# Kernel tuning notes

Measured on AMD Instinct MI355X. Metric: run time of the kernel, lower is better.

## Reference

```python
import jax, jax.numpy as jnp
import numpy as np

D = 64
N = 262144


def _stack_four(A, B, C, Dm):
    return jnp.block([[A, B], [C, Dm]])


def setup_inputs() -> dict:
    key = jax.random.key(0)
    # Z: (2d+1, n+1) in-context prompt matrix
    Z = jax.random.normal(key, (2 * D + 1, N + 1), dtype=jnp.float32)
    # P: zeros with P[-1,-1] = 1 (selects last row)
    P = jnp.zeros((2 * D + 1, 2 * D + 1), dtype=jnp.float32).at[-1, -1].set(1.0)
    # Q: block matrix built from M1, M2, B as in TFLayer.__init__
    I = jnp.eye(D, dtype=jnp.float32)
    O = jnp.zeros((D, D), dtype=jnp.float32)
    M1 = _stack_four(-I, I, O, O)
    M2 = -M1
    Bm = _stack_four(I, O, O, O)  # C = eye(d), so C.T = I
    A = M2.T @ Bm @ M1            # (2d, 2d)
    Q = jnp.zeros((2 * D + 1, 2 * D + 1), dtype=jnp.float32).at[: 2 * D, : 2 * D].set(A)
    return {"Z": Z, "P": P, "Q": Q}


def reference(Z, P, Q):
    # next_Z = Z + (1/n) * P @ Z @ M @ Z.T @ Q @ Z
    # M = eye(n+1) with M[-1,-1] = 0, i.e. right-mult by M zeroes the last
    # column. We never materialize the (n+1, n+1) identity.
    n = Z.shape[1] - 1
    PZ = P @ Z                         # (2d+1, n+1)
    PZM = PZ.at[:, -1].set(0.0)        # apply M: zero last column
    S = PZM @ Z.T                      # (2d+1, 2d+1) -- the only big contraction
    upd = (S @ Q) @ Z                  # (2d+1, n+1)
    return Z + upd / n
```

## Files before the change

### kernel.cpp

```cpp
#include <hip/hip_runtime.h>

#define DD      64
#define ROWS    129
#define NCOLS   262145
#define NDOT    262144
#define DOTROWS 128
#define CHUNK   2048
#define NCHUNK  128

__global__ void k_dot(const float* __restrict__ Z, float* __restrict__ partials) {
    const int row   = blockIdx.x & (DOTROWS - 1);
    const int chunk = blockIdx.x >> 7;
    const long base = (long)chunk * CHUNK;
    const float* zr = Z + (long)row * NCOLS + base;
    const float* zl = Z + (long)128 * NCOLS + base;
    const int tid = threadIdx.x;

    float acc = 0.f;
#pragma unroll
    for (int k = 0; k < CHUNK / 256; ++k) {
        const int c = tid + k * 256;
        acc = fmaf(zr[c], zl[c], acc);
    }
#pragma unroll
    for (int off = 32; off; off >>= 1) acc += __shfl_down(acc, off, 64);
    __shared__ float s[4];
    if ((tid & 63) == 0) s[tid >> 6] = acc;
    __syncthreads();
    if (tid == 0) {
        partials[(long)row * NCHUNK + chunk] = s[0] + s[1] + s[2] + s[3];
    }
}

__global__ void k_matvec(const float* __restrict__ partials,
                         const float* __restrict__ Q,
                         float* __restrict__ t) {
    __shared__ float v[DOTROWS];
    const int tid = threadIdx.x;
    float s = 0.f;
    for (int c = 0; c < NCHUNK; ++c) s += partials[(long)tid * NCHUNK + c];
    v[tid] = s;
    __syncthreads();
    float acc = 0.f;
#pragma unroll 8
    for (int m = 0; m < DOTROWS; ++m) acc = fmaf(v[m], Q[m * ROWS + tid], acc);
    t[tid] = acc * (1.0f / (float)NDOT);
}

__global__ void k_update(const float* __restrict__ Z,
                         const float* __restrict__ t,
                         float* __restrict__ out) {
    __shared__ float ts[DOTROWS];
    const int tid = threadIdx.x;
    if (tid < DOTROWS) ts[tid] = t[tid];
    __syncthreads();

    const long c = (long)blockIdx.x * blockDim.x + tid;
    if (c >= NCOLS) return;

    float acc = 0.f;
#pragma unroll 8
    for (int j = 0; j < DOTROWS; ++j) {
        const float val = Z[(long)j * NCOLS + c];
        out[(long)j * NCOLS + c] = val;
        acc = fmaf(ts[j], val, acc);
    }
    const float zl = Z[(long)128 * NCOLS + c];
    out[(long)128 * NCOLS + c] = zl + acc;
}

extern "C" void kernel_launch(void* const* d_in, const int* in_sizes, int n_in,
                              void* d_out, int out_size, void* d_ws, size_t ws_size,
                              hipStream_t stream) {
    const float* Z = (const float*)d_in[0];
    const float* Q = (const float*)d_in[2];
    float* out = (float*)d_out;

    float* partials = (float*)d_ws;
    float* t        = partials + DOTROWS * NCHUNK;

    k_dot<<<DOTROWS * NCHUNK, 256, 0, stream>>>(Z, partials);
    k_matvec<<<1, DOTROWS, 0, stream>>>(partials, Q, t);
    k_update<<<(NCOLS + 255) / 256, 256, 0, stream>>>(Z, t, out);
}
```

Measured before the change: 280.2 us.

## Fuse identity-row copy into dot pass and parallelize matvec across blocks

```diff
diff --git a/kernel.cpp b/kernel.cpp
--- a/kernel.cpp
+++ b/kernel.cpp
@@ -8,20 +8,38 @@
 #define CHUNK   2048
 #define NCHUNK  128
 
-__global__ void k_dot(const float* __restrict__ Z, float* __restrict__ partials) {
+__global__ __launch_bounds__(256) void k_dot_copy(const float* __restrict__ Z,
+                                                  float* __restrict__ out,
+                                                  float* __restrict__ partials) {
     const int row   = blockIdx.x & (DOTROWS - 1);
     const int chunk = blockIdx.x >> 7;
     const long base = (long)chunk * CHUNK;
     const float* zr = Z + (long)row * NCOLS + base;
-    const float* zl = Z + (long)128 * NCOLS + base;
+    const float* zl = Z + (long)DOTROWS * NCOLS + base;
+    float* orow     = out + (long)row * NCOLS + base;
     const int tid = threadIdx.x;
+
+    __shared__ float szl[CHUNK];
+    const float4* zl4 = (const float4*)zl;
+#pragma unroll
+    for (int k = 0; k < CHUNK / 4 / 256; ++k) {
+        ((float4*)szl)[tid + k * 256] = zl4[tid + k * 256];
+    }
+    __syncthreads();
 
     float acc = 0.f;
 #pragma unroll
     for (int k = 0; k < CHUNK / 256; ++k) {
         const int c = tid + k * 256;
-        acc = fmaf(zr[c], zl[c], acc);
+        const float v = zr[c];
+        __builtin_nontemporal_store(v, &orow[c]);
+        acc = fmaf(v, szl[c], acc);
     }
+    if (chunk == NCHUNK - 1 && tid == 255) {
+        __builtin_nontemporal_store(Z[(long)row * NCOLS + NDOT],
+                                    &out[(long)row * NCOLS + NDOT]);
+    }
+
 #pragma unroll
     for (int off = 32; off; off >>= 1) acc += __shfl_down(acc, off, 64);
     __shared__ float s[4];
@@ -32,41 +50,44 @@
     }
 }
 
-__global__ void k_matvec(const float* __restrict__ partials,
-                         const float* __restrict__ Q,
-                         float* __restrict__ t) {
-    __shared__ float v[DOTROWS];
+__global__ __launch_bounds__(256) void k_matvec(const float* __restrict__ partials,
+                                                const float* __restrict__ Q,
+                                                float* __restrict__ t) {
+    const int j   = blockIdx.x;
     const int tid = threadIdx.x;
-    float s = 0.f;
-    for (int c = 0; c < NCHUNK; ++c) s += partials[(long)tid * NCHUNK + c];
-    v[tid] = s;
+    float acc = 0.f;
+#pragma unroll
+    for (int k = 0; k < (DOTROWS * NCHUNK) / 256; ++k) {
+        const int idx = tid + k * 256;
+        const int m   = idx >> 7;
+        acc = fmaf(partials[idx], Q[m * ROWS + j], acc);
+    }
+#pragma unroll
+    for (int off = 32; off; off >>= 1) acc += __shfl_down(acc, off, 64);
+    __shared__ float s[4];
+    if ((tid & 63) == 0) s[tid >> 6] = acc;
     __syncthreads();
-    float acc = 0.f;
-#pragma unroll 8
-    for (int m = 0; m < DOTROWS; ++m) acc = fmaf(v[m], Q[m * ROWS + tid], acc);
-    t[tid] = acc * (1.0f / (float)NDOT);
+    if (tid == 0) t[j] = (s[0] + s[1] + s[2] + s[3]) * (1.0f / (float)NDOT);
 }
 
-__global__ void k_update(const float* __restrict__ Z,
-                         const float* __restrict__ t,
-                         float* __restrict__ out) {
+__global__ __launch_bounds__(256) void k_row128(const float* __restrict__ Z,
+                                               const float* __restrict__ t,
+                                               float* __restrict__ out) {
     __shared__ float ts[DOTROWS];
     const int tid = threadIdx.x;
     if (tid < DOTROWS) ts[tid] = t[tid];
     __syncthreads();
 
-    const long c = (long)blockIdx.x * blockDim.x + tid;
+    const long c = (long)blockIdx.x * 256 + tid;
     if (c >= NCOLS) return;
 
+    const float* zp = Z + c;
     float acc = 0.f;
 #pragma unroll 8
     for (int j = 0; j < DOTROWS; ++j) {
-        const float val = Z[(long)j * NCOLS + c];
-        out[(long)j * NCOLS + c] = val;
-        acc = fmaf(ts[j], val, acc);
+        acc = fmaf(ts[j], zp[(long)j * NCOLS], acc);
     }
-    const float zl = Z[(long)128 * NCOLS + c];
-    out[(long)128 * NCOLS + c] = zl + acc;
+    out[(long)DOTROWS * NCOLS + c] = Z[(long)DOTROWS * NCOLS + c] + acc;
 }
 
 extern "C" void kernel_launch(void* const* d_in, const int* in_sizes, int n_in,
@@ -79,7 +100,7 @@
     float* partials = (float*)d_ws;
     float* t        = partials + DOTROWS * NCHUNK;
 
-    k_dot<<<DOTROWS * NCHUNK, 256, 0, stream>>>(Z, partials);
-    k_matvec<<<1, DOTROWS, 0, stream>>>(partials, Q, t);
-    k_update<<<(NCOLS + 255) / 256, 256, 0, stream>>>(Z, t, out);
+    k_dot_copy<<<DOTROWS * NCHUNK, 256, 0, stream>>>(Z, out, partials);
+    k_matvec<<<DOTROWS, 256, 0, stream>>>(partials, Q, t);
+    k_row128<<<(NCOLS + 255) / 256, 256, 0, stream>>>(Z, t, out);
 }
```

Result: no change. 276.0 us (-1.5%).

## Fuse copy of first 128 rows into the dot pass with vectorized flat traversal

Applied to the files above, without the earlier changes.

```diff
diff --git a/kernel.cpp b/kernel.cpp
--- a/kernel.cpp
+++ b/kernel.cpp
@@ -2,71 +2,117 @@
 
 #define DD      64
 #define ROWS    129
-#define NCOLS   262145
+#define NCOLS   262145u
 #define NDOT    262144
 #define DOTROWS 128
-#define CHUNK   2048
-#define NCHUNK  128
+#define FLATEND (128u * NCOLS)
+#define SPAN    4096u
+#define NBLK    ((FLATEND + SPAN - 1u) / SPAN)
 
-__global__ void k_dot(const float* __restrict__ Z, float* __restrict__ partials) {
-    const int row   = blockIdx.x & (DOTROWS - 1);
-    const int chunk = blockIdx.x >> 7;
-    const long base = (long)chunk * CHUNK;
-    const float* zr = Z + (long)row * NCOLS + base;
-    const float* zl = Z + (long)128 * NCOLS + base;
+typedef float f32x4 __attribute__((ext_vector_type(4)));
+
+__global__ __launch_bounds__(256) void k_dot_copy(const float* __restrict__ Z,
+                                                  float* __restrict__ out,
+                                                  float* __restrict__ partials) {
+    const unsigned b  = blockIdx.x;
+    const unsigned f0 = b * SPAN;
+    const unsigned r0 = f0 / NCOLS;
+    const unsigned fB = (r0 + 1u) * NCOLS;
+    const float* __restrict__ zl = Z + (unsigned long)DOTROWS * NCOLS;
     const int tid = threadIdx.x;
 
-    float acc = 0.f;
+    float accA = 0.f, accB = 0.f;
 #pragma unroll
-    for (int k = 0; k < CHUNK / 256; ++k) {
-        const int c = tid + k * 256;
-        acc = fmaf(zr[c], zl[c], acc);
+    for (int k = 0; k < 4; ++k) {
+        const unsigned f = f0 + ((unsigned)(tid + k * 256) << 2);
+        if (f < FLATEND) {
+            const f32x4 v = *(const f32x4*)(Z + f);
+            *(f32x4*)(out + f) = v;
+            if (f >= fB || f + 3u < fB) {
+                const bool hi = (f >= fB);
+                const unsigned c0 = f - (hi ? fB : fB - NCOLS);
+                float zlv[4];
+                __builtin_memcpy(zlv, zl + c0, 16);
+                const unsigned fm = (fB - 1u) - f;
+                if (fm < 4u) zlv[fm] = 0.f;
+                float s = v.x * zlv[0];
+                s = fmaf(v.y, zlv[1], s);
+                s = fmaf(v.z, zlv[2], s);
+                s = fmaf(v.w, zlv[3], s);
+                if (hi) accB += s; else accA += s;
+            } else {
+#pragma unroll
+                for (int e = 0; e < 4; ++e) {
+                    const unsigned fe = f + (unsigned)e;
+                    const bool hi = (fe >= fB);
+                    const unsigned col = fe - (hi ? fB : fB - NCOLS);
+                    const float ve = (e == 0) ? v.x : (e == 1) ? v.y : (e == 2) ? v.z : v.w;
+                    float p = ve * zl[col];
+                    if (fe == fB - 1u) p = 0.f;
+                    if (hi) accB += p; else accA += p;
+                }
+            }
+        }
     }
+
 #pragma unroll
-    for (int off = 32; off; off >>= 1) acc += __shfl_down(acc, off, 64);
-    __shared__ float s[4];
-    if ((tid & 63) == 0) s[tid >> 6] = acc;
+    for (int off = 32; off; off >>= 1) {
+        accA += __shfl_down(accA, off, 64);
+        accB += __shfl_down(accB, off, 64);
+    }
+    __shared__ float wA[4], wB[4];
+    if ((tid & 63) == 0) { wA[tid >> 6] = accA; wB[tid >> 6] = accB; }
     __syncthreads();
     if (tid == 0) {
-        partials[(long)row * NCHUNK + chunk] = s[0] + s[1] + s[2] + s[3];
+        partials[2u * b + 0u] = wA[0] + wA[1] + wA[2] + wA[3];
+        partials[2u * b + 1u] = wB[0] + wB[1] + wB[2] + wB[3];
     }
 }
 
-__global__ void k_matvec(const float* __restrict__ partials,
-                         const float* __restrict__ Q,
-                         float* __restrict__ t) {
+__global__ __launch_bounds__(256) void k_matvec(const float* __restrict__ partials,
+                                                const float* __restrict__ Q,
+                                                float* __restrict__ t) {
     __shared__ float v[DOTROWS];
     const int tid = threadIdx.x;
-    float s = 0.f;
-    for (int c = 0; c < NCHUNK; ++c) s += partials[(long)tid * NCHUNK + c];
-    v[tid] = s;
+    if (tid < DOTROWS) v[tid] = 0.f;
     __syncthreads();
-    float acc = 0.f;
+    for (unsigned i = tid; i < 2u * NBLK; i += 256u) {
+        const unsigned blk = i >> 1;
+        const unsigned r0  = (blk * SPAN) / NCOLS;
+        const unsigned row = r0 + (i & 1u);
+        if (row < DOTROWS) atomicAdd(&v[row], partials[i]);
+    }
+    __syncthreads();
+    if (tid < DOTROWS) {
+        float acc = 0.f;
 #pragma unroll 8
-    for (int m = 0; m < DOTROWS; ++m) acc = fmaf(v[m], Q[m * ROWS + tid], acc);
-    t[tid] = acc * (1.0f / (float)NDOT);
+        for (int m = 0; m < DOTROWS; ++m) acc = fmaf(v[m], Q[m * ROWS + tid], acc);
+        t[tid] = acc * (1.0f / (float)NDOT);
+    }
 }
 
-__global__ void k_update(const float* __restrict__ Z,
-                         const float* __restrict__ t,
-                         float* __restrict__ out) {
+__global__ __launch_bounds__(256) void k_row128(const float* __restrict__ Z,
+                                               const float* __restrict__ t,
+                                               float* __restrict__ out) {
     __shared__ float ts[DOTROWS];
     const int tid = threadIdx.x;
     if (tid < DOTROWS) ts[tid] = t[tid];
     __syncthreads();
 
-    const long c = (long)blockIdx.x * blockDim.x + tid;
-    if (c >= NCOLS) return;
+    const long c = (long)blockIdx.x * 256 + tid;
+    if (c >= (long)NCOLS) return;
 
-    float acc = 0.f;
+    const float* zp = Z + c;
+    float a0 = 0.f, a1 = 0.f, a2 = 0.f, a3 = 0.f;
 #pragma unroll 8
-    for (int j = 0; j < DOTROWS; ++j) {
-        const float val = Z[(long)j * NCOLS + c];
-        out[(long)j * NCOLS + c] = val;
-        acc = fmaf(ts[j], val, acc);
+    for (int j = 0; j < DOTROWS; j += 4) {
+        a0 = fmaf(ts[j + 0], zp[(long)(j + 0) * NCOLS], a0);
+        a1 = fmaf(ts[j + 1], zp[(long)(j + 1) * NCOLS], a1);
+        a2 = fmaf(ts[j + 2], zp[(long)(j + 2) * NCOLS], a2);
+        a3 = fmaf(ts[j + 3], zp[(long)(j + 3) * NCOLS], a3);
     }
-    const float zl = Z[(long)128 * NCOLS + c];
-    out[(long)128 * NCOLS + c] = zl + acc;
+    out[(long)DOTROWS * NCOLS + c] =
+        Z[(long)DOTROWS * NCOLS + c] + ((a0 + a1) + (a2 + a3));
 }
 
 extern "C" void kernel_launch(void* const* d_in, const int* in_sizes, int n_in,
@@ -77,9 +123,9 @@
     float* out = (float*)d_out;
 
     float* partials = (float*)d_ws;
-    float* t        = partials + DOTROWS * NCHUNK;
+    float* t        = partials + 2u * NBLK;
 
-    k_dot<<<DOTROWS * NCHUNK, 256, 0, stream>>>(Z, partials);
-    k_matvec<<<1, DOTROWS, 0, stream>>>(partials, Q, t);
-    k_update<<<(NCOLS + 255) / 256, 256, 0, stream>>>(Z, t, out);
+    k_dot_copy<<<NBLK, 256, 0, stream>>>(Z, out, partials);
+    k_matvec<<<1, 256, 0, stream>>>(partials, Q, t);
+    k_row128<<<((int)NCOLS + 255) / 256, 256, 0, stream>>>(Z, t, out);
 }
```

Measured after the change: 303.8 us. +8.4%, slower.
